# Performance work log

Hardware: AMD Instinct MI355X
Metric: run time of the kernel (lower is better)

Reference implementation:

```python
import jax, jax.numpy as jnp
import numpy as np

H = 768      # hidden_size (MambaConfig default)
DI = 500     # intermediate_size (overridden)
N = 16       # state_size
R = 48       # time_step_rank = ceil(768/16)
K = 4        # conv_kernel
LYR = 5      # num_hidden_layers
EPS = 1e-5   # layer_norm_epsilon
B, L, IN = 8, 1024, 4096


def _rmsnorm(x, w):
    v = jnp.mean(jnp.square(x), axis=-1, keepdims=True)
    return x * jax.lax.rsqrt(v + EPS) * w


def _mixer(x, in_proj, conv_w, conv_b, x_proj, dt_w, dt_b, A_log, Dp, out_w):
    # x: [B, L, H]
    proj = x @ in_proj                       # [B, L, 2*DI]
    u, gate = jnp.split(proj, 2, axis=-1)
    # causal depthwise conv1d (torch Conv1d padding=K-1, sliced to L)
    up = jnp.pad(u, ((0, 0), (K - 1, 0), (0, 0)))
    conv = conv_b
    for k in range(K):
        conv = conv + up[:, k:k + x.shape[1], :] * conv_w[:, k]
    u = jax.nn.silu(conv)                    # [B, L, DI]
    ssm = u @ x_proj                         # [B, L, R + 2N]
    dt, Bm, Cm = ssm[..., :R], ssm[..., R:R + N], ssm[..., R + N:]
    dt = jax.nn.softplus(dt @ dt_w + dt_b)   # [B, L, DI]
    A = -jnp.exp(A_log)                      # [DI, N]
    dA = jnp.exp(dt[..., None] * A)          # [B, L, DI, N]
    dBu = dt[..., None] * Bm[:, :, None, :] * u[..., None]  # [B, L, DI, N]

    def step(h, xs):
        dA_t, dBu_t, C_t = xs
        h = dA_t * h + dBu_t                 # [B, DI, N]
        y = jnp.einsum('bdn,bn->bd', h, C_t)
        return h, y

    h0 = jnp.zeros((u.shape[0], DI, N), dtype=u.dtype)
    _, ys = jax.lax.scan(step, h0, (dA.transpose(1, 0, 2, 3),
                                    dBu.transpose(1, 0, 2, 3),
                                    Cm.transpose(1, 0, 2)))
    y = ys.transpose(1, 0, 2)                # [B, L, DI]
    y = y + u * Dp
    y = y * jax.nn.silu(gate)
    return y @ out_w                         # [B, L, H]


def setup_inputs() -> dict:
    key = jax.random.key(0)
    ks = jax.random.split(key, 12)
    s = 0.02
    inputs = jax.random.normal(ks[0], (B, L, IN), jnp.float32)
    W_down = jax.random.normal(ks[1], (IN, H), jnp.float32) * s
    in_proj = jax.random.normal(ks[2], (LYR, H, 2 * DI), jnp.float32) * s
    conv_w = jax.random.normal(ks[3], (LYR, DI, K), jnp.float32) * 0.1
    conv_b = jnp.zeros((LYR, DI), jnp.float32)
    x_proj = jax.random.normal(ks[4], (LYR, DI, R + 2 * N), jnp.float32) * s
    dt_w = jax.random.normal(ks[5], (LYR, R, DI), jnp.float32) * s
    dt_b = jax.random.normal(ks[6], (LYR, DI), jnp.float32) * 0.1
    A_log = jnp.broadcast_to(jnp.log(jnp.arange(1, N + 1, dtype=jnp.float32)),
                             (LYR, DI, N)).copy()
    D_param = jnp.ones((LYR, DI), jnp.float32)
    out_w = jax.random.normal(ks[7], (LYR, DI, H), jnp.float32) * s
    norm_w = jnp.ones((LYR, H), jnp.float32)
    norm_f_w = jnp.ones((H,), jnp.float32)
    W_cls = jax.random.normal(ks[8], (H, 1), jnp.float32) * s
    return dict(inputs=inputs, W_down=W_down, in_proj=in_proj, conv_w=conv_w,
                conv_b=conv_b, x_proj=x_proj, dt_w=dt_w, dt_b=dt_b,
                A_log=A_log, D_param=D_param, out_w=out_w, norm_w=norm_w,
                norm_f_w=norm_f_w, W_cls=W_cls)


def reference(inputs, W_down, in_proj, conv_w, conv_b, x_proj, dt_w, dt_b,
              A_log, D_param, out_w, norm_w, norm_f_w, W_cls):
    x = inputs @ W_down                      # down projection [B, L, H]
    for i in range(LYR):
        x = x + _mixer(_rmsnorm(x, norm_w[i]), in_proj[i], conv_w[i],
                       conv_b[i], x_proj[i], dt_w[i], dt_b[i], A_log[i],
                       D_param[i], out_w[i])
    x = _rmsnorm(x, norm_f_w)
    out = x[:, -1]                           # last token [B, H]
    logits = out @ W_cls                     # [B, 1]
    return logits
```

## Files before the change

### kernel.cpp

```cpp
#include <hip/hip_runtime.h>
#include <hip/hip_bf16.h>

#define BATCH 8
#define SEQL 1024
#define INDIM 4096
#define HDIM 768
#define DI 500
#define NSTATE 16
#define RRANK 48
#define KCONV 4
#define NLAYER 5
#define BL (BATCH * SEQL)

typedef __attribute__((ext_vector_type(8))) short bf16x8;
typedef __attribute__((ext_vector_type(4))) float f32x4;

__device__ __forceinline__ void gl_lds16(const void* g, void* l) {
  __builtin_amdgcn_global_load_lds(
      (const __attribute__((address_space(1))) void*)g,
      (__attribute__((address_space(3))) void*)l, 16, 0, 0);
}

__device__ __forceinline__ unsigned short f2bf(float v) {
  return __hip_bfloat16_raw(__float2bfloat16(v)).x;
}
__device__ __forceinline__ float bf2f(unsigned short h) {
  unsigned int u = ((unsigned int)h) << 16;
  float f;
  memcpy(&f, &u, 4);
  return f;
}

template <int CTRL>
__device__ __forceinline__ float ror_add(float x) {
  int r = __builtin_amdgcn_update_dpp(0, __float_as_int(x), CTRL, 0xf, 0xf,
                                      true);
  return x + __int_as_float(r);
}

template <int EPI>
__global__ __launch_bounds__(256) void gemm_mfma(
    const short* __restrict__ A, const short* __restrict__ Bt,
    float* __restrict__ C, const float* __restrict__ bias,
    unsigned short* __restrict__ D0, unsigned short* __restrict__ D1,
    int M, int N, int K, int lda, int ldb, int ldc) {
  __shared__ short As[3][128 * 32];
  __shared__ short Bs[3][128 * 32];
  const int tid = threadIdx.x;
  const int w = tid >> 6, lane = tid & 63;

  const int gx = gridDim.x;
  const int nwg = gx * gridDim.y;
  int flat = blockIdx.y * gx + blockIdx.x;
  flat = (flat & 7) * (nwg >> 3) + (flat >> 3);
  const int m0 = (flat / gx) * 128, n0 = (flat % gx) * 128;

  const int wr = w >> 1, wc = w & 1;
  f32x4 acc[4][4] = {};

  const int srow = tid >> 2;
  const int cpos = tid & 3;
  const int sc = (cpos ^ ((srow >> 1) & 3)) * 8;
  const short* ga0 = A + (size_t)(m0 + srow) * lda + sc;
  const short* ga1 = A + (size_t)(m0 + 64 + srow) * lda + sc;
  const short* gb0 = Bt + (size_t)(n0 + srow) * ldb + sc;
  const short* gb1 = Bt + (size_t)(n0 + 64 + srow) * ldb + sc;
  const int lr = lane & 15, kb = lane >> 4;
  const int kbx = (kb ^ ((lr >> 1) & 3)) * 8;

  auto stage = [&](int buf, int k0) {
    gl_lds16(ga0 + k0, &As[buf][w * 512]);
    gl_lds16(ga1 + k0, &As[buf][2048 + w * 512]);
    gl_lds16(gb0 + k0, &Bs[buf][w * 512]);
    gl_lds16(gb1 + k0, &Bs[buf][2048 + w * 512]);
  };
  auto compute = [&](int buf) {
    bf16x8 af[4], bfr[4];
#pragma unroll
    for (int i = 0; i < 4; ++i) {
      af[i] = *(const bf16x8*)&As[buf][(wr * 64 + i * 16 + lr) * 32 + kbx];
      bfr[i] = *(const bf16x8*)&Bs[buf][(wc * 64 + i * 16 + lr) * 32 + kbx];
    }
#pragma unroll
    for (int i = 0; i < 4; ++i)
#pragma unroll
      for (int j = 0; j < 4; ++j)
        acc[i][j] = __builtin_amdgcn_mfma_f32_16x16x32_bf16(af[i], bfr[j],
                                                            acc[i][j], 0, 0, 0);
  };

  const int nk = K >> 5;
  stage(0, 0);
  if (nk > 1) stage(1, 32);
  int cur = 0;
  for (int t = 0; t < nk; ++t) {
    if (t + 1 < nk)
      asm volatile("s_waitcnt vmcnt(4)" ::: "memory");
    else
      asm volatile("s_waitcnt vmcnt(0)" ::: "memory");
    __builtin_amdgcn_s_barrier();
    __builtin_amdgcn_sched_barrier(0);
    compute(cur);
    if (t + 2 < nk) {
      int nb = cur + 2;
      if (nb >= 3) nb -= 3;
      stage(nb, (t + 2) * 32);
    }
    ++cur;
    if (cur == 3) cur = 0;
  }

#pragma unroll
  for (int i = 0; i < 4; ++i) {
    const int row = m0 + wr * 64 + i * 16 + (lane >> 4) * 4;
#pragma unroll
    for (int j = 0; j < 4; ++j) {
      const int col = n0 + wc * 64 + j * 16 + (lane & 15);
      if (EPI == 3) {
        if (col < N) {
          float4 v4;
#pragma unroll
          for (int r = 0; r < 4; ++r) {
            float v = acc[i][j][r] + bias[col];
            ((float*)&v4)[r] = (v > 15.f) ? v : log1pf(expf(v));
          }
          const int bb = row >> 10, tt = row & 1023;
          *(float4*)&C[((size_t)bb * DI + col) * 1024 + tt] = v4;
        }
      } else if (EPI == 4) {
#pragma unroll
        for (int r = 0; r < 4; ++r) {
          unsigned short h = f2bf(acc[i][j][r]);
          size_t rr = (size_t)(row + r);
          if (col < DI)
            D0[rr * 512 + col] = h;
          else
            D1[rr * 512 + (col - DI)] = h;
        }
      } else if (EPI == 5) {
#pragma unroll
        for (int r = 0; r < 4; ++r) {
          float v = acc[i][j][r];
          size_t rr = (size_t)(row + r);
          if (col < 64) D0[rr * 64 + col] = f2bf(col < RRANK ? v : 0.f);
          if (col >= RRANK && col < 64) C[rr * 32 + 2 * (col - RRANK)] = v;
          if (col >= 64 && col < 80) C[rr * 32 + 2 * (col - 64) + 1] = v;
        }
      } else {
        if (col < N) {
#pragma unroll
          for (int r = 0; r < 4; ++r) {
            float v = acc[i][j][r];
            size_t idx = (size_t)(row + r) * ldc + col;
            if (EPI == 1) v += C[idx];
            C[idx] = v;
          }
        }
      }
    }
  }
}

__global__ __launch_bounds__(256) void convert_cast(
    const float* __restrict__ src, __hip_bfloat16* __restrict__ dst, long n) {
  long i = ((long)blockIdx.x * 256 + threadIdx.x) * 4;
  if (i >= n) return;
  float4 v = *(const float4*)(src + i);
  dst[i + 0] = __float2bfloat16(v.x);
  dst[i + 1] = __float2bfloat16(v.y);
  dst[i + 2] = __float2bfloat16(v.z);
  dst[i + 3] = __float2bfloat16(v.w);
}

__global__ __launch_bounds__(256) void convert_wT(
    const float* __restrict__ src, __hip_bfloat16* __restrict__ dst, int K,
    int N, int Kpad, int Npad, long src_lstride, long dst_lstride) {
  int idx = blockIdx.x * 256 + threadIdx.x;
  int per = Kpad * Npad;
  if (idx >= per) return;
  const float* s = src + (long)blockIdx.y * src_lstride;
  __hip_bfloat16* d = dst + (long)blockIdx.y * dst_lstride;
  int n = idx / Kpad, k = idx % Kpad;
  float v = (k < K && n < N) ? s[(long)k * N + n] : 0.f;
  d[idx] = __float2bfloat16(v);
}

__device__ __forceinline__ float block_sum256(float v, float* sm) {
#pragma unroll
  for (int off = 32; off > 0; off >>= 1) v += __shfl_down(v, off, 64);
  int wid = threadIdx.x >> 6;
  if ((threadIdx.x & 63) == 0) sm[wid] = v;
  __syncthreads();
  float t = sm[0] + sm[1] + sm[2] + sm[3];
  __syncthreads();
  return t;
}

__global__ __launch_bounds__(256) void rmsnorm_kernel(
    const float* __restrict__ X, const float* __restrict__ w,
    __hip_bfloat16* __restrict__ XN) {
  __shared__ float sm[4];
  const long row = blockIdx.x;
  const float* x = X + row * HDIM;
  float vals[3];
  float s = 0.f;
#pragma unroll
  for (int j = 0; j < 3; ++j) {
    vals[j] = x[threadIdx.x + j * 256];
    s += vals[j] * vals[j];
  }
  float tot = block_sum256(s, sm);
  float scale = rsqrtf(tot / (float)HDIM + 1e-5f);
#pragma unroll
  for (int j = 0; j < 3; ++j) {
    int c = threadIdx.x + j * 256;
    XN[row * HDIM + c] = __float2bfloat16(vals[j] * scale * w[c]);
  }
}

__global__ __launch_bounds__(256) void conv_fused_kernel(
    const unsigned short* __restrict__ Uraw, const float* __restrict__ cw,
    const float* __restrict__ cb, unsigned short* __restrict__ Ubf,
    unsigned short* __restrict__ Ut, int layer) {
  __shared__ unsigned short tin[35][33];
  __shared__ unsigned short tout[32][33];
  const int d0 = blockIdx.x * 32, t0 = blockIdx.y * 32, b = blockIdx.z;
  const int tx = threadIdx.x & 31, ty = threadIdx.x >> 5;
#pragma unroll
  for (int r = 0; r < 5; ++r) {
    int tr = ty + r * 8;
    if (tr < 35) {
      int t = t0 + tr - (KCONV - 1);
      tin[tr][tx] =
          (t >= 0) ? Uraw[((size_t)b * 1024 + t) * 512 + d0 + tx] : 0;
    }
  }
  __syncthreads();
  const int d = d0 + tx;
  float w0 = 0.f, w1 = 0.f, w2 = 0.f, w3 = 0.f, bias = 0.f;
  if (d < DI) {
    const float* w = cw + ((size_t)layer * DI + d) * KCONV;
    w0 = w[0]; w1 = w[1]; w2 = w[2]; w3 = w[3];
    bias = cb[layer * DI + d];
  }
#pragma unroll
  for (int r = 0; r < 4; ++r) {
    const int tt = ty + r * 8;
    unsigned short h = 0;
    if (d < DI) {
      float a = bias + w0 * bf2f(tin[tt][tx]) + w1 * bf2f(tin[tt + 1][tx]) +
                w2 * bf2f(tin[tt + 2][tx]) + w3 * bf2f(tin[tt + 3][tx]);
      h = f2bf(a / (1.f + expf(-a)));
    }
    tout[tt][tx] = h;
    Ubf[((size_t)b * 1024 + t0 + tt) * 512 + d] = h;
  }
  __syncthreads();
#pragma unroll
  for (int r = 0; r < 4; ++r) {
    const int dd = ty + r * 8;
    Ut[((size_t)b * 512 + d0 + dd) * 1024 + t0 + tx] = tout[tx][dd];
  }
}

__global__ __launch_bounds__(256) void y_gate_kernel(
    const unsigned short* __restrict__ Yt, const unsigned short* __restrict__ G,
    unsigned short* __restrict__ Ybf) {
  __shared__ unsigned short tile[32][33];
  const int d0 = blockIdx.x * 32, t0 = blockIdx.y * 32, b = blockIdx.z;
  const int tx = threadIdx.x & 31, ty = threadIdx.x >> 5;
#pragma unroll
  for (int r = 0; r < 4; ++r) {
    int d = d0 + ty + r * 8;
    tile[ty + r * 8][tx] =
        (d < DI) ? Yt[((size_t)b * 512 + d) * 1024 + t0 + tx]
                 : (unsigned short)0;
  }
  __syncthreads();
#pragma unroll
  for (int r = 0; r < 4; ++r) {
    size_t row = (size_t)b * 1024 + t0 + ty + r * 8;
    int d = d0 + tx;
    float yv = 0.f;
    if (d < DI) {
      float y = bf2f(tile[tx][ty + r * 8]);
      float g = bf2f(G[row * 512 + d]);
      yv = y * (g / (1.f + expf(-g)));
    }
    Ybf[row * 512 + d] = f2bf(yv);
  }
}

__global__ __launch_bounds__(512) void scan_kernel(
    const float* __restrict__ DTt, const unsigned short* __restrict__ Ut,
    const float* __restrict__ BC, const float* __restrict__ A_log,
    const float* __restrict__ Dparam, unsigned short* __restrict__ Yt,
    int layer) {
  __shared__ float2 sdtu[4][1036];
  __shared__ float s_ap[8][4][16];
  __shared__ float s_h0[8][4][16];
  __shared__ float s_hi[8][4][16];
  const int orig = blockIdx.x;
  const int blk = (orig & 7) * 125 + (orig >> 3);
  const int b = blk / 125;
  const int d0 = (blk - b * 125) * 4;
  const int tid = threadIdx.x;
  const int c = tid >> 6;
  const int lane = tid & 63;
  const int dl = lane >> 4;
  const int n = lane & 15;
  const int d = d0 + dl;

#pragma unroll
  for (int k = 0; k < 8; ++k) {
    int x = tid + k * 512;
    int dd = x >> 10, t = x & 1023;
    float dtv = DTt[((size_t)b * DI + d0 + dd) * 1024 + t];
    float uv = bf2f(Ut[((size_t)b * 512 + d0 + dd) * 1024 + t]);
    sdtu[dd][t] = make_float2(dtv, uv);
  }
  __syncthreads();

  const float An2 =
      -expf(A_log[((size_t)layer * DI + d) * NSTATE + n]) * 1.44269504f;
  const float Dp = Dparam[layer * DI + d];
  const int t0 = c * 128;
  const float2* sb = &sdtu[dl][t0];
  const float2* bcp = (const float2*)(BC + ((size_t)b * 1024 + t0) * 32) + n;

  {
    float h = 0.f, cum = 0.f;
#pragma unroll 8
    for (int s = 0; s < 128; ++s) {
      float2 du = sb[s];
      float a = exp2f(du.x * An2);
      cum += du.x;
      h = a * h + du.x * du.y * bcp[s * 16].x;
    }
    s_ap[c][dl][n] = exp2f(An2 * cum);
    s_h0[c][dl][n] = h;
  }
  __syncthreads();

  if (tid < 64) {
    float hi = 0.f;
    for (int cc = 0; cc < 8; ++cc) {
      s_hi[cc][dl][n] = hi;
      hi = s_ap[cc][dl][n] * hi + s_h0[cc][dl][n];
    }
  }
  __syncthreads();

  {
    float h = s_hi[c][dl][n];
    unsigned short* yp = Yt + ((size_t)b * 512 + d) * 1024 + t0;
#pragma unroll 4
    for (int s = 0; s < 128; s += 2) {
      float2 du0 = sb[s], du1 = sb[s + 1];
      float2 v0 = bcp[s * 16], v1 = bcp[(s + 1) * 16];
      float a0 = exp2f(du0.x * An2);
      h = a0 * h + du0.x * du0.y * v0.x;
      float p0 = h * v0.y;
      float a1 = exp2f(du1.x * An2);
      h = a1 * h + du1.x * du1.y * v1.x;
      float p1 = h * v1.y;
      p0 = ror_add<0x128>(p0);
      p1 = ror_add<0x128>(p1);
      p0 = ror_add<0x124>(p0);
      p1 = ror_add<0x124>(p1);
      p0 = ror_add<0x122>(p0);
      p1 = ror_add<0x122>(p1);
      p0 = ror_add<0x121>(p0);
      p1 = ror_add<0x121>(p1);
      if (n == 0) {
        float y0 = p0 + du0.y * Dp;
        float y1 = p1 + du1.y * Dp;
        unsigned int pk =
            (unsigned int)f2bf(y0) | ((unsigned int)f2bf(y1) << 16);
        *(unsigned int*)(yp + s) = pk;
      }
    }
  }
}

__global__ __launch_bounds__(256) void final_kernel(
    const float* __restrict__ X, const float* __restrict__ nfw,
    const float* __restrict__ Wcls, float* __restrict__ out) {
  __shared__ float sm[4];
  const int b = blockIdx.x;
  const long row = (long)b * SEQL + (SEQL - 1);
  const float* x = X + row * HDIM;
  float vals[3];
  float s = 0.f;
#pragma unroll
  for (int j = 0; j < 3; ++j) {
    vals[j] = x[threadIdx.x + j * 256];
    s += vals[j] * vals[j];
  }
  float tot = block_sum256(s, sm);
  float scale = rsqrtf(tot / (float)HDIM + 1e-5f);
  float dot = 0.f;
#pragma unroll
  for (int j = 0; j < 3; ++j) {
    int c = threadIdx.x + j * 256;
    dot += vals[j] * scale * nfw[c] * Wcls[c];
  }
  float td = block_sum256(dot, sm);
  if (threadIdx.x == 0) out[b] = td;
}

extern "C" void kernel_launch(void* const* d_in, const int* in_sizes, int n_in,
                              void* d_out, int out_size, void* d_ws,
                              size_t ws_size, hipStream_t stream) {
  const float* inputs  = (const float*)d_in[0];
  const float* W_down  = (const float*)d_in[1];
  const float* in_proj = (const float*)d_in[2];
  const float* conv_w  = (const float*)d_in[3];
  const float* conv_b  = (const float*)d_in[4];
  const float* x_proj  = (const float*)d_in[5];
  const float* dt_w    = (const float*)d_in[6];
  const float* dt_b    = (const float*)d_in[7];
  const float* A_log   = (const float*)d_in[8];
  const float* D_param = (const float*)d_in[9];
  const float* out_w   = (const float*)d_in[10];
  const float* norm_w  = (const float*)d_in[11];
  const float* norm_fw = (const float*)d_in[12];
  const float* W_cls   = (const float*)d_in[13];
  float* out = (float*)d_out;

  char* ws = (char*)d_ws;
  __hip_bfloat16* Abf   = (__hip_bfloat16*)(ws + 0);
  __hip_bfloat16* Wdbf  = (__hip_bfloat16*)(ws + 67108864);
  __hip_bfloat16* XNbf  = (__hip_bfloat16*)(ws + 0);
  unsigned short* Yt    = (unsigned short*)(ws + 0);
  float*          DTt   = (float*)(ws + 12582912);
  unsigned short* Uraw  = (unsigned short*)(ws + 28966912);
  unsigned short* Ybf   = (unsigned short*)(ws + 28966912);
  unsigned short* Gate  = (unsigned short*)(ws + 37355520);
  unsigned short* Ubf   = (unsigned short*)(ws + 45744128);
  unsigned short* Ut    = (unsigned short*)(ws + 54132736);
  float*          BC    = (float*)(ws + 62521344);
  __hip_bfloat16* SSMbf = (__hip_bfloat16*)(ws + 66715648);
  float*          X     = (float*)(ws + 73400320);
  __hip_bfloat16* inpbf = (__hip_bfloat16*)(ws + 98566144);
  __hip_bfloat16* xpbf  = (__hip_bfloat16*)(ws + 106430464);
  __hip_bfloat16* dtwbf = (__hip_bfloat16*)(ws + 107085824);
  __hip_bfloat16* outwbf= (__hip_bfloat16*)(ws + 107413504);

  convert_cast<<<(long)BL * 4096 / 4 / 256, 256, 0, stream>>>(inputs, Abf,
                                                              (long)BL * 4096);
  convert_wT<<<dim3((768 * 4096 + 255) / 256, 1), 256, 0, stream>>>(
      W_down, Wdbf, 4096, 768, 4096, 768, 0, 0);
  convert_wT<<<dim3((768 * 1024 + 255) / 256, NLAYER), 256, 0, stream>>>(
      in_proj, inpbf, 768, 1000, 768, 1024, (long)HDIM * 1000, 768 * 1024);
  convert_wT<<<dim3((128 * 512 + 255) / 256, NLAYER), 256, 0, stream>>>(
      x_proj, xpbf, 500, 80, 512, 128, (long)DI * 80, 128 * 512);
  convert_wT<<<dim3((512 * 64 + 255) / 256, NLAYER), 256, 0, stream>>>(
      dt_w, dtwbf, 48, 500, 64, 512, (long)RRANK * DI, 512 * 64);
  convert_wT<<<dim3((768 * 512 + 255) / 256, NLAYER), 256, 0, stream>>>(
      out_w, outwbf, 500, 768, 512, 768, (long)DI * HDIM, 768 * 512);

  gemm_mfma<0><<<dim3(768 / 128, BL / 128), 256, 0, stream>>>(
      (const short*)Abf, (const short*)Wdbf, X, nullptr, nullptr, nullptr, BL,
      HDIM, INDIM, INDIM, INDIM, HDIM);

  for (int i = 0; i < NLAYER; ++i) {
    rmsnorm_kernel<<<BL, 256, 0, stream>>>(X, norm_w + i * HDIM, XNbf);
    gemm_mfma<4><<<dim3(1024 / 128, BL / 128), 256, 0, stream>>>(
        (const short*)XNbf, (const short*)(inpbf + (long)i * 768 * 1024),
        nullptr, nullptr, Uraw, Gate, BL, 1000, HDIM, HDIM, HDIM, 0);
    conv_fused_kernel<<<dim3(16, 32, 8), 256, 0, stream>>>(Uraw, conv_w,
                                                           conv_b, Ubf, Ut, i);
    gemm_mfma<5><<<dim3(1, BL / 128), 256, 0, stream>>>(
        (const short*)Ubf, (const short*)(xpbf + (long)i * 128 * 512), BC,
        nullptr, (unsigned short*)SSMbf, nullptr, BL, 80, 512, 512, 512, 0);
    gemm_mfma<3><<<dim3(512 / 128, BL / 128), 256, 0, stream>>>(
        (const short*)SSMbf, (const short*)(dtwbf + (long)i * 512 * 64), DTt,
        dt_b + i * DI, nullptr, nullptr, BL, DI, 64, 64, 64, 0);
    scan_kernel<<<1000, 512, 0, stream>>>(DTt, Ut, BC, A_log, D_param, Yt, i);
    y_gate_kernel<<<dim3(16, 32, 8), 256, 0, stream>>>(Yt, Gate, Ybf);
    gemm_mfma<1><<<dim3(768 / 128, BL / 128), 256, 0, stream>>>(
        (const short*)Ybf, (const short*)(outwbf + (long)i * 768 * 512), X,
        nullptr, nullptr, nullptr, BL, HDIM, 512, 512, 512, HDIM);
  }

  final_kernel<<<BATCH, 256, 0, stream>>>(X, norm_fw, W_cls, out);
}
```

Measured before the change: 1.122 ms.

## Fold dt projection into x_proj weights and split-K the down projection

```diff
diff --git a/kernel.cpp b/kernel.cpp
--- a/kernel.cpp
+++ b/kernel.cpp
@@ -49,22 +49,29 @@
   const int tid = threadIdx.x;
   const int w = tid >> 6, lane = tid & 63;
 
+  if (EPI == 6) {
+    A += (size_t)blockIdx.z * 512 * 64;
+    Bt += (size_t)blockIdx.z * 512 * 64;
+    D0 += (size_t)blockIdx.z * 640 * 512;
+  }
+  const int koff = (EPI == 7) ? blockIdx.z * K : 0;
+
   const int gx = gridDim.x;
   const int nwg = gx * gridDim.y;
   int flat = blockIdx.y * gx + blockIdx.x;
   flat = (flat & 7) * (nwg >> 3) + (flat >> 3);
   const int m0 = (flat / gx) * 128, n0 = (flat % gx) * 128;
 
-  const int wr = w >> 1, wc = w & 1;
+  const int wr = (w >> 1), wc = w & 1;
   f32x4 acc[4][4] = {};
 
   const int srow = tid >> 2;
   const int cpos = tid & 3;
   const int sc = (cpos ^ ((srow >> 1) & 3)) * 8;
-  const short* ga0 = A + (size_t)(m0 + srow) * lda + sc;
-  const short* ga1 = A + (size_t)(m0 + 64 + srow) * lda + sc;
-  const short* gb0 = Bt + (size_t)(n0 + srow) * ldb + sc;
-  const short* gb1 = Bt + (size_t)(n0 + 64 + srow) * ldb + sc;
+  const short* ga0 = A + (size_t)(m0 + srow) * lda + sc + koff;
+  const short* ga1 = A + (size_t)(m0 + 64 + srow) * lda + sc + koff;
+  const short* gb0 = Bt + (size_t)(n0 + srow) * ldb + sc + koff;
+  const short* gb1 = Bt + (size_t)(n0 + 64 + srow) * ldb + sc + koff;
   const int lr = lane & 15, kb = lane >> 4;
   const int kbx = (kb ^ ((lr >> 1) & 3)) * 8;
 
@@ -116,18 +123,7 @@
 #pragma unroll
     for (int j = 0; j < 4; ++j) {
       const int col = n0 + wc * 64 + j * 16 + (lane & 15);
-      if (EPI == 3) {
-        if (col < N) {
-          float4 v4;
-#pragma unroll
-          for (int r = 0; r < 4; ++r) {
-            float v = acc[i][j][r] + bias[col];
-            ((float*)&v4)[r] = (v > 15.f) ? v : log1pf(expf(v));
-          }
-          const int bb = row >> 10, tt = row & 1023;
-          *(float4*)&C[((size_t)bb * DI + col) * 1024 + tt] = v4;
-        }
-      } else if (EPI == 4) {
+      if (EPI == 4) {
 #pragma unroll
         for (int r = 0; r < 4; ++r) {
           unsigned short h = f2bf(acc[i][j][r]);
@@ -138,21 +134,37 @@
             D1[rr * 512 + (col - DI)] = h;
         }
       } else if (EPI == 5) {
-#pragma unroll
-        for (int r = 0; r < 4; ++r) {
-          float v = acc[i][j][r];
-          size_t rr = (size_t)(row + r);
-          if (col < 64) D0[rr * 64 + col] = f2bf(col < RRANK ? v : 0.f);
-          if (col >= RRANK && col < 64) C[rr * 32 + 2 * (col - RRANK)] = v;
-          if (col >= 64 && col < 80) C[rr * 32 + 2 * (col - 64) + 1] = v;
+        if (col < 32) {
+          const int o = (col < 16) ? 2 * col : 2 * (col - 16) + 1;
+#pragma unroll
+          for (int r = 0; r < 4; ++r)
+            C[(size_t)(row + r) * 32 + o] = acc[i][j][r];
+        } else if (col < 532) {
+          float* DTtp = (float*)D0;
+          float4 v4;
+#pragma unroll
+          for (int r = 0; r < 4; ++r) {
+            float v = acc[i][j][r] + bias[col - 32];
+            ((float*)&v4)[r] = (v > 15.f) ? v : log1pf(expf(v));
+          }
+          const int bb = row >> 10, tt = row & 1023;
+          *(float4*)&DTtp[((size_t)bb * DI + (col - 32)) * 1024 + tt] = v4;
         }
+      } else if (EPI == 6) {
+#pragma unroll
+        for (int r = 0; r < 4; ++r)
+          D0[(size_t)(32 + row + r) * 512 + col] = f2bf(acc[i][j][r]);
+      } else if (EPI == 7) {
+#pragma unroll
+        for (int r = 0; r < 4; ++r)
+          unsafeAtomicAdd(&C[(size_t)(row + r) * ldc + col], acc[i][j][r]);
       } else {
         if (col < N) {
 #pragma unroll
           for (int r = 0; r < 4; ++r) {
             float v = acc[i][j][r];
             size_t idx = (size_t)(row + r) * ldc + col;
-            if (EPI == 1) v += C[idx];
+            v += C[idx];
             C[idx] = v;
           }
         }
@@ -183,6 +195,30 @@
   int n = idx / Kpad, k = idx % Kpad;
   float v = (k < K && n < N) ? s[(long)k * N + n] : 0.f;
   d[idx] = __float2bfloat16(v);
+}
+
+__global__ __launch_bounds__(256) void convert_pad_xpdt(
+    const float* __restrict__ xp, __hip_bfloat16* __restrict__ dst) {
+  int idx = blockIdx.x * 256 + threadIdx.x;
+  if (idx >= 512 * 64) return;
+  int k = idx >> 6, r = idx & 63;
+  float v = (k < DI && r < RRANK)
+                ? xp[(size_t)blockIdx.y * DI * 80 + k * 80 + r]
+                : 0.f;
+  dst[(size_t)blockIdx.y * 512 * 64 + idx] = __float2bfloat16(v);
+}
+
+__global__ __launch_bounds__(256) void bc_rows_kernel(
+    const float* __restrict__ xp, __hip_bfloat16* __restrict__ Wfull) {
+  int idx = blockIdx.x * 256 + threadIdx.x;
+  if (idx >= 32 * 512) return;
+  int n = idx >> 9, k = idx & 511;
+  float v = 0.f;
+  if (k < DI) {
+    int src_col = (n < 16) ? (RRANK + n) : (RRANK + NSTATE + (n - 16));
+    v = xp[(size_t)blockIdx.y * DI * 80 + k * 80 + src_col];
+  }
+  Wfull[(size_t)blockIdx.y * 640 * 512 + idx] = __float2bfloat16(v);
 }
 
 __device__ __forceinline__ float block_sum256(float v, float* sm) {
@@ -440,12 +476,12 @@
   unsigned short* Ubf   = (unsigned short*)(ws + 45744128);
   unsigned short* Ut    = (unsigned short*)(ws + 54132736);
   float*          BC    = (float*)(ws + 62521344);
-  __hip_bfloat16* SSMbf = (__hip_bfloat16*)(ws + 66715648);
   float*          X     = (float*)(ws + 73400320);
   __hip_bfloat16* inpbf = (__hip_bfloat16*)(ws + 98566144);
-  __hip_bfloat16* xpbf  = (__hip_bfloat16*)(ws + 106430464);
   __hip_bfloat16* dtwbf = (__hip_bfloat16*)(ws + 107085824);
   __hip_bfloat16* outwbf= (__hip_bfloat16*)(ws + 107413504);
+  __hip_bfloat16* xpdt  = (__hip_bfloat16*)(ws + 111345664);
+  __hip_bfloat16* Wfull = (__hip_bfloat16*)(ws + 111673344);
 
   convert_cast<<<(long)BL * 4096 / 4 / 256, 256, 0, stream>>>(inputs, Abf,
                                                               (long)BL * 4096);
@@ -453,16 +489,22 @@
       W_down, Wdbf, 4096, 768, 4096, 768, 0, 0);
   convert_wT<<<dim3((768 * 1024 + 255) / 256, NLAYER), 256, 0, stream>>>(
       in_proj, inpbf, 768, 1000, 768, 1024, (long)HDIM * 1000, 768 * 1024);
-  convert_wT<<<dim3((128 * 512 + 255) / 256, NLAYER), 256, 0, stream>>>(
-      x_proj, xpbf, 500, 80, 512, 128, (long)DI * 80, 128 * 512);
   convert_wT<<<dim3((512 * 64 + 255) / 256, NLAYER), 256, 0, stream>>>(
       dt_w, dtwbf, 48, 500, 64, 512, (long)RRANK * DI, 512 * 64);
   convert_wT<<<dim3((768 * 512 + 255) / 256, NLAYER), 256, 0, stream>>>(
       out_w, outwbf, 500, 768, 512, 768, (long)DI * HDIM, 768 * 512);
-
-  gemm_mfma<0><<<dim3(768 / 128, BL / 128), 256, 0, stream>>>(
+  convert_pad_xpdt<<<dim3(128, NLAYER), 256, 0, stream>>>(x_proj, xpdt);
+
+  hipMemsetAsync(Wfull, 0, (size_t)NLAYER * 640 * 512 * 2, stream);
+  bc_rows_kernel<<<dim3(64, NLAYER), 256, 0, stream>>>(x_proj, Wfull);
+  gemm_mfma<6><<<dim3(4, 4, NLAYER), 256, 0, stream>>>(
+      (const short*)dtwbf, (const short*)xpdt, nullptr, nullptr,
+      (unsigned short*)Wfull, nullptr, 512, 512, 64, 64, 64, 0);
+
+  hipMemsetAsync(X, 0, (size_t)BL * HDIM * 4, stream);
+  gemm_mfma<7><<<dim3(768 / 128, BL / 128, 2), 256, 0, stream>>>(
       (const short*)Abf, (const short*)Wdbf, X, nullptr, nullptr, nullptr, BL,
-      HDIM, INDIM, INDIM, INDIM, HDIM);
+      HDIM, INDIM / 2, INDIM, INDIM, HDIM);
 
   for (int i = 0; i < NLAYER; ++i) {
     rmsnorm_kernel<<<BL, 256, 0, stream>>>(X, norm_w + i * HDIM, XNbf);
@@ -471,12 +513,10 @@
         nullptr, nullptr, Uraw, Gate, BL, 1000, HDIM, HDIM, HDIM, 0);
     conv_fused_kernel<<<dim3(16, 32, 8), 256, 0, stream>>>(Uraw, conv_w,
                                                            conv_b, Ubf, Ut, i);
-    gemm_mfma<5><<<dim3(1, BL / 128), 256, 0, stream>>>(
-        (const short*)Ubf, (const short*)(xpbf + (long)i * 128 * 512), BC,
-        nullptr, (unsigned short*)SSMbf, nullptr, BL, 80, 512, 512, 512, 0);
-    gemm_mfma<3><<<dim3(512 / 128, BL / 128), 256, 0, stream>>>(
-        (const short*)SSMbf, (const short*)(dtwbf + (long)i * 512 * 64), DTt,
-        dt_b + i * DI, nullptr, nullptr, BL, DI, 64, 64, 64, 0);
+    gemm_mfma<5><<<dim3(5, BL / 128), 256, 0, stream>>>(
+        (const short*)Ubf, (const short*)(Wfull + (size_t)i * 640 * 512), BC,
+        dt_b + i * DI, (unsigned short*)DTt, nullptr, BL, 532, 512, 512, 512,
+        0);
     scan_kernel<<<1000, 512, 0, stream>>>(DTt, Ut, BC, A_log, D_param, Yt, i);
     y_gate_kernel<<<dim3(16, 32, 8), 256, 0, stream>>>(Yt, Gate, Ybf);
     gemm_mfma<1><<<dim3(768 / 128, BL / 128), 256, 0, stream>>>(
```

Measured after the change: 1.176 ms. +4.8%, slower.

## Split-K the down-projection GEMM and fuse partial-sum reduction into first RMSNorm

Applied to the files above, without the earlier changes.

```diff
diff --git a/kernel.cpp b/kernel.cpp
--- a/kernel.cpp
+++ b/kernel.cpp
@@ -49,22 +49,24 @@
   const int tid = threadIdx.x;
   const int w = tid >> 6, lane = tid & 63;
 
+  const int koff = (EPI == 7) ? blockIdx.z * K : 0;
+
   const int gx = gridDim.x;
   const int nwg = gx * gridDim.y;
   int flat = blockIdx.y * gx + blockIdx.x;
   flat = (flat & 7) * (nwg >> 3) + (flat >> 3);
   const int m0 = (flat / gx) * 128, n0 = (flat % gx) * 128;
 
-  const int wr = w >> 1, wc = w & 1;
+  const int wr = (w >> 1), wc = w & 1;
   f32x4 acc[4][4] = {};
 
   const int srow = tid >> 2;
   const int cpos = tid & 3;
   const int sc = (cpos ^ ((srow >> 1) & 3)) * 8;
-  const short* ga0 = A + (size_t)(m0 + srow) * lda + sc;
-  const short* ga1 = A + (size_t)(m0 + 64 + srow) * lda + sc;
-  const short* gb0 = Bt + (size_t)(n0 + srow) * ldb + sc;
-  const short* gb1 = Bt + (size_t)(n0 + 64 + srow) * ldb + sc;
+  const short* ga0 = A + (size_t)(m0 + srow) * lda + sc + koff;
+  const short* ga1 = A + (size_t)(m0 + 64 + srow) * lda + sc + koff;
+  const short* gb0 = Bt + (size_t)(n0 + srow) * ldb + sc + koff;
+  const short* gb1 = Bt + (size_t)(n0 + 64 + srow) * ldb + sc + koff;
   const int lr = lane & 15, kb = lane >> 4;
   const int kbx = (kb ^ ((lr >> 1) & 3)) * 8;
 
@@ -146,6 +148,13 @@
           if (col >= RRANK && col < 64) C[rr * 32 + 2 * (col - RRANK)] = v;
           if (col >= 64 && col < 80) C[rr * 32 + 2 * (col - 64) + 1] = v;
         }
+      } else if (EPI == 7) {
+        float* dst = blockIdx.z ? (float*)D0 : C;
+        if (col < N) {
+#pragma unroll
+          for (int r = 0; r < 4; ++r)
+            dst[(size_t)(row + r) * ldc + col] = acc[i][j][r];
+        }
       } else {
         if (col < N) {
 #pragma unroll
@@ -197,8 +206,9 @@
 }
 
 __global__ __launch_bounds__(256) void rmsnorm_kernel(
-    const float* __restrict__ X, const float* __restrict__ w,
-    __hip_bfloat16* __restrict__ XN) {
+    const float* __restrict__ X, const float* __restrict__ X2,
+    const float* __restrict__ w, __hip_bfloat16* __restrict__ XN,
+    float* __restrict__ Xout) {
   __shared__ float sm[4];
   const long row = blockIdx.x;
   const float* x = X + row * HDIM;
@@ -206,7 +216,9 @@
   float s = 0.f;
 #pragma unroll
   for (int j = 0; j < 3; ++j) {
-    vals[j] = x[threadIdx.x + j * 256];
+    int c = threadIdx.x + j * 256;
+    vals[j] = x[c];
+    if (X2) vals[j] += X2[row * HDIM + c];
     s += vals[j] * vals[j];
   }
   float tot = block_sum256(s, sm);
@@ -214,6 +226,7 @@
 #pragma unroll
   for (int j = 0; j < 3; ++j) {
     int c = threadIdx.x + j * 256;
+    if (X2) Xout[row * HDIM + c] = vals[j];
     XN[row * HDIM + c] = __float2bfloat16(vals[j] * scale * w[c]);
   }
 }
@@ -446,6 +459,8 @@
   __hip_bfloat16* xpbf  = (__hip_bfloat16*)(ws + 106430464);
   __hip_bfloat16* dtwbf = (__hip_bfloat16*)(ws + 107085824);
   __hip_bfloat16* outwbf= (__hip_bfloat16*)(ws + 107413504);
+  float*          Xb    = (float*)(ws + 111345664);
+  const bool splitk = ws_size >= 136511488ull;
 
   convert_cast<<<(long)BL * 4096 / 4 / 256, 256, 0, stream>>>(inputs, Abf,
                                                               (long)BL * 4096);
@@ -460,12 +475,22 @@
   convert_wT<<<dim3((768 * 512 + 255) / 256, NLAYER), 256, 0, stream>>>(
       out_w, outwbf, 500, 768, 512, 768, (long)DI * HDIM, 768 * 512);
 
-  gemm_mfma<0><<<dim3(768 / 128, BL / 128), 256, 0, stream>>>(
-      (const short*)Abf, (const short*)Wdbf, X, nullptr, nullptr, nullptr, BL,
-      HDIM, INDIM, INDIM, INDIM, HDIM);
+  if (splitk) {
+    gemm_mfma<7><<<dim3(768 / 128, BL / 128, 2), 256, 0, stream>>>(
+        (const short*)Abf, (const short*)Wdbf, X, nullptr,
+        (unsigned short*)Xb, nullptr, BL, HDIM, INDIM / 2, INDIM, INDIM,
+        HDIM);
+  } else {
+    gemm_mfma<0><<<dim3(768 / 128, BL / 128), 256, 0, stream>>>(
+        (const short*)Abf, (const short*)Wdbf, X, nullptr, nullptr, nullptr,
+        BL, HDIM, INDIM, INDIM, INDIM, HDIM);
+  }
 
   for (int i = 0; i < NLAYER; ++i) {
-    rmsnorm_kernel<<<BL, 256, 0, stream>>>(X, norm_w + i * HDIM, XNbf);
+    const float* x2 = (i == 0 && splitk) ? Xb : nullptr;
+    float* xout = (i == 0 && splitk) ? X : nullptr;
+    rmsnorm_kernel<<<BL, 256, 0, stream>>>(X, x2, norm_w + i * HDIM, XNbf,
+                                           xout);
     gemm_mfma<4><<<dim3(1024 / 128, BL / 128), 256, 0, stream>>>(
         (const short*)XNbf, (const short*)(inpbf + (long)i * 768 * 1024),
         nullptr, nullptr, Uraw, Gate, BL, 1000, HDIM, HDIM, HDIM, 0);
```

After: 1.141 ms. Within noise of the previous version (+1.7%).
